# Kernel optimization log

Measured on AMD Instinct MI355X. Metric: run time of the kernel, lower is better.

Reference implementation:

```python
import jax, jax.numpy as jnp
import numpy as np

BITS = 4
GROUP = 128
IN_F = 4096
OUT_F = 4096
N_TOK = 8192
N_STAGES = 4
QMAX = 2 ** BITS - 1  # affine (sym=False)


def _round_ste(x):
    return x + jax.lax.stop_gradient(jnp.round(x) - x)


def _clamp_ste(x, lo, hi):
    return x + jax.lax.stop_gradient(jnp.clip(x, lo, hi) - x)


def apply_rotation(x, pairs, theta, group_size):
    # x: [N, H]; pairs: [R, H] int (per-group index pairs in [0, group_size));
    # theta: [R, H//2]
    n, h = x.shape
    g = h // group_size
    half = group_size // 2
    offsets = (jnp.arange(g, dtype=jnp.int32) * group_size)[:, None]  # [G,1]
    pair_view = pairs.reshape(pairs.shape[0], g, half, 2)
    theta_view = theta.reshape(theta.shape[0], g, half)
    out = x
    for r in range(pairs.shape[0]):  # small fixed number of rotation stages
        idx_i = (pair_view[r, :, :, 0] + offsets).reshape(-1)  # [H//2]
        idx_j = (pair_view[r, :, :, 1] + offsets).reshape(-1)
        xi = out[:, idx_i]  # [N, H//2]
        xj = out[:, idx_j]
        c = jnp.cos(theta_view[r]).reshape(-1)[None, :]
        s = jnp.sin(theta_view[r]).reshape(-1)[None, :]
        out = out.at[:, idx_i].set(xi * c + xj * s).at[:, idx_j].set(-xi * s + xj * c)
    return out


def quant_dequant_affine_ste(w, scale, zero_point_float, group_size):
    # pseudo_quantize_dequant with sym=False, use_ste=True
    view = w.reshape(-1, group_size)
    s = _clamp_ste(scale, 1e-5, 1e5)
    rzp = _clamp_ste(-_round_ste(zero_point_float), 0.0, float(QMAX))
    q = _round_ste(view / s) + rzp
    q = _clamp_ste(q, 0.0, float(QMAX))
    return ((q - rzp) * s).reshape(w.shape)


def setup_inputs() -> dict:
    key = jax.random.key(0)
    k1, k2, k3, k4 = jax.random.split(key, 4)
    x = jax.random.normal(k1, (N_TOK, IN_F), dtype=jnp.float32)
    weight = jax.random.normal(k2, (OUT_F, IN_F), dtype=jnp.float32) * 0.02
    bias = jax.random.normal(k3, (OUT_F,), dtype=jnp.float32) * 0.01
    channel_scales = jnp.ones((IN_F,), dtype=jnp.float32)
    theta = jax.random.normal(k4, (N_STAGES, IN_F // 2), dtype=jnp.float32) * 0.05
    # per-group pair permutations: each stage/group is a permutation of [0, GROUP)
    rng = np.random.default_rng(0)
    g = IN_F // GROUP
    pairs_np = np.stack([
        np.concatenate([rng.permutation(GROUP) for _ in range(g)])
        for _ in range(N_STAGES)
    ]).astype(np.int32)  # [R, IN_F]
    pairs = jnp.asarray(pairs_np)
    # affine qparams from initial (theta=0, scales=1) transformed weight == weight
    view = weight.reshape(-1, GROUP)
    min_val = view.min(axis=1, keepdims=True)
    max_val = view.max(axis=1, keepdims=True)
    q_scale = jnp.clip(max_val - min_val, 1e-5, None) / QMAX
    q_zero_point = min_val / q_scale
    theta_mask = jnp.ones((N_STAGES, IN_F // 2), dtype=bool)
    return {"x": x, "weight": weight, "bias": bias,
            "channel_scales": channel_scales, "theta": theta,
            "q_scale": q_scale, "q_zero_point": q_zero_point,
            "pairs": pairs, "theta_mask": theta_mask}


def reference(x, weight, bias, channel_scales, theta, q_scale, q_zero_point, pairs, theta_mask):
    # transformed_weight(): scale input channels then group-wise Givens rotate
    w_scaled = weight * channel_scales[None, :]
    w_t = apply_rotation(w_scaled, pairs, theta, GROUP)
    # STE pseudo quantize-dequantize in the transformed domain
    w_q = quant_dequant_affine_ste(w_t, q_scale, q_zero_point, GROUP)
    # inverse rotation back to the original input domain, undo channel scales
    w_back = apply_rotation(w_q, pairs[::-1], -theta[::-1], GROUP) / channel_scales[None, :]
    return x @ w_back.T + bias[None, :]
```

## Files before the change

kernel.cpp:

```cpp
#include <hip/hip_runtime.h>
#include <hip/hip_bf16.h>
#include <math.h>

#define IN_F    4096
#define OUT_F   4096
#define N_TOK   8192
#define GROUP   128
#define NSTAGE  4
#define NPAIRS  2048
#define QMAXF   15.0

typedef unsigned short u16;
typedef __bf16 bf16x8 __attribute__((ext_vector_type(8)));
typedef float  f32x4  __attribute__((ext_vector_type(4)));

struct alignas(8) U16x4 { u16 x, y, z, w; };

__device__ __forceinline__ u16 f2bf(float f) {
    unsigned u = __float_as_uint(f);
    unsigned r = (u + 0x7fffu + ((u >> 16) & 1u)) >> 16;
    return (u16)r;
}

__device__ __forceinline__ void gl_lds16(const void* g, void* l) {
    __builtin_amdgcn_global_load_lds(
        (const __attribute__((address_space(1))) void*)g,
        (__attribute__((address_space(3))) void*)l,
        16, 0, 0);
}

__global__ void make_tabs(const float* __restrict__ theta,
                          double* __restrict__ ctab, double* __restrict__ stab) {
    int i = blockIdx.x * 256 + threadIdx.x;
    if (i < NSTAGE * NPAIRS) {
        double t = (double)theta[i];
        ctab[i] = cos(t);
        stab[i] = sin(t);
    }
}

__global__ __launch_bounds__(256) void build_w(
    const float* __restrict__ weight, const float* __restrict__ cs,
    const float* __restrict__ qs, const float* __restrict__ qzp,
    const int* __restrict__ pairs,
    const double* __restrict__ ctab, const double* __restrict__ stab,
    u16* __restrict__ wb) {
    __shared__ double gbuf[4][GROUP];
    const int wave = threadIdx.x >> 6, l = threadIdx.x & 63;
    const int task = blockIdx.x * 4 + wave;
    const int o = task >> 5, g = task & 31;
    double* gb = gbuf[wave];
    const int e0 = g * GROUP;

    float2 wv = *(const float2*)(weight + (size_t)o * IN_F + e0 + 2 * l);
    float2 cv = *(const float2*)(cs + e0 + 2 * l);
    gb[2 * l]     = (double)wv.x * (double)cv.x;
    gb[2 * l + 1] = (double)wv.y * (double)cv.y;
    __builtin_amdgcn_wave_barrier();

    const int2* prs = (const int2*)pairs;

    for (int r = 0; r < NSTAGE; ++r) {
        int2 p = prs[r * (IN_F / 2) + g * 64 + l];
        double c = ctab[r * NPAIRS + g * 64 + l];
        double s = stab[r * NPAIRS + g * 64 + l];
        double xi = gb[p.x], xj = gb[p.y];
        __builtin_amdgcn_wave_barrier();
        gb[p.x] =  xi * c + xj * s;
        gb[p.y] = -xi * s + xj * c;
        __builtin_amdgcn_wave_barrier();
    }

    {
        double s   = fmin(fmax((double)qs[o * 32 + g], 1e-5), 1e5);
        double rzp = fmin(fmax(-rint((double)qzp[o * 32 + g]), 0.0), QMAXF);
#pragma unroll
        for (int e = 2 * l; e <= 2 * l + 1; ++e) {
            double q = rint(gb[e] / s) + rzp;
            q = fmin(fmax(q, 0.0), QMAXF);
            gb[e] = (q - rzp) * s;
        }
        __builtin_amdgcn_wave_barrier();
    }

    for (int r = NSTAGE - 1; r >= 0; --r) {
        int2 p = prs[r * (IN_F / 2) + g * 64 + l];
        double c = ctab[r * NPAIRS + g * 64 + l];
        double s = stab[r * NPAIRS + g * 64 + l];
        double xi = gb[p.x], xj = gb[p.y];
        __builtin_amdgcn_wave_barrier();
        gb[p.x] = xi * c - xj * s;
        gb[p.y] = xi * s + xj * c;
        __builtin_amdgcn_wave_barrier();
    }

    unsigned lo = f2bf((float)(gb[2 * l]     / (double)cv.x));
    unsigned hi = f2bf((float)(gb[2 * l + 1] / (double)cv.y));
    *(unsigned*)(wb + (size_t)o * IN_F + e0 + 2 * l) = lo | (hi << 16);
}

__global__ void cast_x(const float* __restrict__ x, u16* __restrict__ xb) {
    size_t i = ((size_t)blockIdx.x * 256 + threadIdx.x) * 4;
    float4 v = *(const float4*)(x + i);
    U16x4 o;
    o.x = f2bf(v.x); o.y = f2bf(v.y); o.z = f2bf(v.z); o.w = f2bf(v.w);
    *(U16x4*)(xb + i) = o;
}

__global__ __launch_bounds__(256) void gemm_bt(
    const u16* __restrict__ A, const u16* __restrict__ B,
    const float* __restrict__ bias, float* __restrict__ C) {
    constexpr int K = IN_F;
    constexpr int N = OUT_F;
    __shared__ __align__(16) u16 As[128 * 32];
    __shared__ __align__(16) u16 Bs[128 * 32];

    const int tid  = threadIdx.x;
    const int wave = tid >> 6, lane = tid & 63;
    const int ntile = N / 128;
    const int mt = blockIdx.x / ntile, nt = blockIdx.x % ntile;
    const int m0 = mt * 128, n0 = nt * 128;
    const u16* Ab = A + (size_t)m0 * K;
    const u16* Bb = B + (size_t)n0 * K;

    f32x4 acc[4][4];
#pragma unroll
    for (int i = 0; i < 4; ++i)
#pragma unroll
        for (int j = 0; j < 4; ++j) acc[i][j] = (f32x4){0.f, 0.f, 0.f, 0.f};

    const int lrow = lane & 15, lq = lane >> 4;
    const int mw = (wave >> 1) * 64, nw = (wave & 1) * 64;

    const int sc0 = tid;
    const int sc1 = 256 + tid;
    const int srow0 = sc0 >> 2, sgch0 = ((sc0 ^ (srow0 >> 1)) & 3) << 3;
    const int srow1 = sc1 >> 2, sgch1 = ((sc1 ^ (srow1 >> 1)) & 3) << 3;

    for (int k0 = 0; k0 < K; k0 += 32) {
        gl_lds16(Ab + (size_t)srow0 * K + (k0 + sgch0), &As[(wave * 64) * 8]);
        gl_lds16(Ab + (size_t)srow1 * K + (k0 + sgch1), &As[(256 + wave * 64) * 8]);
        gl_lds16(Bb + (size_t)srow0 * K + (k0 + sgch0), &Bs[(wave * 64) * 8]);
        gl_lds16(Bb + (size_t)srow1 * K + (k0 + sgch1), &Bs[(256 + wave * 64) * 8]);
        __syncthreads();

        bf16x8 af[4], bfr[4];
#pragma unroll
        for (int i = 0; i < 4; ++i) {
            int ar = mw + i * 16 + lrow;
            af[i] = *(const bf16x8*)&As[ar * 32 + (((lq ^ (ar >> 1)) & 3) << 3)];
        }
#pragma unroll
        for (int j = 0; j < 4; ++j) {
            int br = nw + j * 16 + lrow;
            bfr[j] = *(const bf16x8*)&Bs[br * 32 + (((lq ^ (br >> 1)) & 3) << 3)];
        }
#pragma unroll
        for (int i = 0; i < 4; ++i)
#pragma unroll
            for (int j = 0; j < 4; ++j)
                acc[i][j] = __builtin_amdgcn_mfma_f32_16x16x32_bf16(
                    af[i], bfr[j], acc[i][j], 0, 0, 0);
        __syncthreads();
    }

#pragma unroll
    for (int i = 0; i < 4; ++i) {
        int rb = m0 + mw + i * 16 + lq * 4;
#pragma unroll
        for (int j = 0; j < 4; ++j) {
            int col = n0 + nw + j * 16 + lrow;
            float bv = bias[col];
#pragma unroll
            for (int r = 0; r < 4; ++r)
                C[(size_t)(rb + r) * N + col] = acc[i][j][r] + bv;
        }
    }
}

extern "C" void kernel_launch(void* const* d_in, const int* in_sizes, int n_in,
                              void* d_out, int out_size, void* d_ws, size_t ws_size,
                              hipStream_t stream) {
    const float* x    = (const float*)d_in[0];
    const float* w    = (const float*)d_in[1];
    const float* bias = (const float*)d_in[2];
    const float* cs   = (const float*)d_in[3];
    const float* th   = (const float*)d_in[4];
    const float* qs   = (const float*)d_in[5];
    const float* qzp  = (const float*)d_in[6];
    const int*   pr   = (const int*)d_in[7];
    float* out = (float*)d_out;

    char* ws = (char*)d_ws;
    double* ctab = (double*)ws;
    double* stab = (double*)(ws + 65536);
    u16*    xb   = (u16*)(ws + 131072);
    u16*    wb   = (u16*)(ws + 131072 + (size_t)N_TOK * IN_F * 2);

    hipLaunchKernelGGL(make_tabs, dim3((NSTAGE * NPAIRS + 255) / 256), dim3(256),
                       0, stream, th, ctab, stab);
    hipLaunchKernelGGL(build_w, dim3(OUT_F * 32 / 4), dim3(256), 0, stream,
                       w, cs, qs, qzp, pr, ctab, stab, wb);
    hipLaunchKernelGGL(cast_x, dim3(N_TOK * IN_F / 4 / 256), dim3(256), 0, stream,
                       x, xb);
    hipLaunchKernelGGL(gemm_bt, dim3((N_TOK / 128) * (OUT_F / 128)), dim3(256),
                       0, stream, xb, wb, bias, out);
}
```

Baseline: 645.2 us.

## Restructure GEMM to 256x256 tiles with 4-stage async LDS pipeline

Rewrites the bf16 GEMM to use 512-thread blocks on 256x256 output tiles, with a four-slot LDS ring that prefetches three k-steps ahead through direct global-to-LDS loads gated by manual vmcnt waits. A single barrier per k-step replaces the two per step used before. It also adds a blockIdx swizzle for L2 locality and raises MFMA priority with setprio. The goal is to hide global load latency and raise arithmetic intensity per block. The cost is a larger LDS footprint (128 KB per block) and more accumulator registers, which may limit occupancy.

```diff
diff --git a/kernel.cpp b/kernel.cpp
--- a/kernel.cpp
+++ b/kernel.cpp
@@ -107,73 +107,97 @@
     *(U16x4*)(xb + i) = o;
 }
 
-__global__ __launch_bounds__(256) void gemm_bt(
+__global__ __launch_bounds__(512, 2) void gemm_bt(
     const u16* __restrict__ A, const u16* __restrict__ B,
     const float* __restrict__ bias, float* __restrict__ C) {
     constexpr int K = IN_F;
     constexpr int N = OUT_F;
-    __shared__ __align__(16) u16 As[128 * 32];
-    __shared__ __align__(16) u16 Bs[128 * 32];
+    constexpr int NS = K / 32;
+    __shared__ __align__(16) u16 As[4][256 * 32];
+    __shared__ __align__(16) u16 Bs[4][256 * 32];
 
     const int tid  = threadIdx.x;
     const int wave = tid >> 6, lane = tid & 63;
-    const int ntile = N / 128;
-    const int mt = blockIdx.x / ntile, nt = blockIdx.x % ntile;
-    const int m0 = mt * 128, n0 = nt * 128;
-    const u16* Ab = A + (size_t)m0 * K;
-    const u16* Bb = B + (size_t)n0 * K;
-
-    f32x4 acc[4][4];
-#pragma unroll
-    for (int i = 0; i < 4; ++i)
+    const int lrow = lane & 15, lq = lane >> 4;
+    const int wm = wave >> 2, wn = wave & 3;
+
+    const int wg = (blockIdx.x & 7) * 64 + (blockIdx.x >> 3);
+    const int mt = wg & 31, nt = wg >> 5;
+    const int m0 = mt * 256, n0 = nt * 256;
+
+    const int srow = tid >> 2;
+    const int gch  = (tid & 3) ^ ((tid >> 3) & 3);
+    const u16* pA0 = A + (size_t)(m0 + srow) * K + gch * 8;
+    const u16* pA1 = pA0 + (size_t)128 * K;
+    const u16* pB0 = B + (size_t)(n0 + srow) * K + gch * 8;
+    const u16* pB1 = pB0 + (size_t)128 * K;
+
+#define STAGE(slot, s) do {                                         \
+        const int ko_ = (s) * 32;                                   \
+        gl_lds16(pA0 + ko_, &As[slot][wave * 512]);                 \
+        gl_lds16(pA1 + ko_, &As[slot][4096 + wave * 512]);          \
+        gl_lds16(pB0 + ko_, &Bs[slot][wave * 512]);                 \
+        gl_lds16(pB1 + ko_, &Bs[slot][4096 + wave * 512]);          \
+    } while (0)
+
+    f32x4 acc[8][4];
+#pragma unroll
+    for (int i = 0; i < 8; ++i)
 #pragma unroll
         for (int j = 0; j < 4; ++j) acc[i][j] = (f32x4){0.f, 0.f, 0.f, 0.f};
 
-    const int lrow = lane & 15, lq = lane >> 4;
-    const int mw = (wave >> 1) * 64, nw = (wave & 1) * 64;
-
-    const int sc0 = tid;
-    const int sc1 = 256 + tid;
-    const int srow0 = sc0 >> 2, sgch0 = ((sc0 ^ (srow0 >> 1)) & 3) << 3;
-    const int srow1 = sc1 >> 2, sgch1 = ((sc1 ^ (srow1 >> 1)) & 3) << 3;
-
-    for (int k0 = 0; k0 < K; k0 += 32) {
-        gl_lds16(Ab + (size_t)srow0 * K + (k0 + sgch0), &As[(wave * 64) * 8]);
-        gl_lds16(Ab + (size_t)srow1 * K + (k0 + sgch1), &As[(256 + wave * 64) * 8]);
-        gl_lds16(Bb + (size_t)srow0 * K + (k0 + sgch0), &Bs[(wave * 64) * 8]);
-        gl_lds16(Bb + (size_t)srow1 * K + (k0 + sgch1), &Bs[(256 + wave * 64) * 8]);
-        __syncthreads();
-
-        bf16x8 af[4], bfr[4];
-#pragma unroll
-        for (int i = 0; i < 4; ++i) {
-            int ar = mw + i * 16 + lrow;
-            af[i] = *(const bf16x8*)&As[ar * 32 + (((lq ^ (ar >> 1)) & 3) << 3)];
-        }
-#pragma unroll
-        for (int j = 0; j < 4; ++j) {
-            int br = nw + j * 16 + lrow;
-            bfr[j] = *(const bf16x8*)&Bs[br * 32 + (((lq ^ (br >> 1)) & 3) << 3)];
-        }
-#pragma unroll
-        for (int i = 0; i < 4; ++i)
-#pragma unroll
-            for (int j = 0; j < 4; ++j)
-                acc[i][j] = __builtin_amdgcn_mfma_f32_16x16x32_bf16(
-                    af[i], bfr[j], acc[i][j], 0, 0, 0);
-        __syncthreads();
-    }
-
-#pragma unroll
-    for (int i = 0; i < 4; ++i) {
-        int rb = m0 + mw + i * 16 + lq * 4;
-#pragma unroll
-        for (int j = 0; j < 4; ++j) {
-            int col = n0 + nw + j * 16 + lrow;
+    STAGE(0, 0); STAGE(1, 1); STAGE(2, 2);
+
+#define BODY(s, VMSTR, DO_STAGE) do {                                          \
+        asm volatile("s_waitcnt " VMSTR);                                      \
+        __builtin_amdgcn_s_barrier();                                          \
+        asm volatile("" ::: "memory");                                         \
+        const u16* as_ = As[(s) & 3];                                          \
+        const u16* bs_ = Bs[(s) & 3];                                          \
+        bf16x8 af[8], bf[4];                                                   \
+        _Pragma("unroll")                                                      \
+        for (int mi = 0; mi < 8; ++mi) {                                       \
+            int ar = wm * 128 + mi * 16 + lrow;                                \
+            af[mi] = *(const bf16x8*)&as_[ar * 32 +                            \
+                                          (((lq ^ (ar >> 1)) & 3) << 3)];      \
+        }                                                                      \
+        _Pragma("unroll")                                                      \
+        for (int nj = 0; nj < 4; ++nj) {                                       \
+            int br = wn * 64 + nj * 16 + lrow;                                 \
+            bf[nj] = *(const bf16x8*)&bs_[br * 32 +                            \
+                                          (((lq ^ (br >> 1)) & 3) << 3)];      \
+        }                                                                      \
+        if (DO_STAGE) STAGE(((s) + 3) & 3, (s) + 3);                           \
+        __builtin_amdgcn_s_setprio(1);                                         \
+        _Pragma("unroll")                                                      \
+        for (int mi = 0; mi < 8; ++mi)                                         \
+            _Pragma("unroll")                                                  \
+            for (int nj = 0; nj < 4; ++nj)                                     \
+                acc[mi][nj] = __builtin_amdgcn_mfma_f32_16x16x32_bf16(         \
+                    af[mi], bf[nj], acc[mi][nj], 0, 0, 0);                     \
+        __builtin_amdgcn_s_setprio(0);                                         \
+        asm volatile("" ::: "memory");                                         \
+    } while (0)
+
+    for (int s = 0; s < NS - 3; ++s)
+        BODY(s, "vmcnt(8)", 1);
+    BODY(NS - 3, "vmcnt(8)", 0);
+    BODY(NS - 2, "vmcnt(4)", 0);
+    BODY(NS - 1, "vmcnt(0)", 0);
+
+#undef BODY
+#undef STAGE
+
+#pragma unroll
+    for (int mi = 0; mi < 8; ++mi) {
+        int rb = m0 + wm * 128 + mi * 16 + lq * 4;
+#pragma unroll
+        for (int nj = 0; nj < 4; ++nj) {
+            int col = n0 + wn * 64 + nj * 16 + lrow;
             float bv = bias[col];
 #pragma unroll
             for (int r = 0; r < 4; ++r)
-                C[(size_t)(rb + r) * N + col] = acc[i][j][r] + bv;
+                C[(size_t)(rb + r) * N + col] = acc[mi][nj][r] + bv;
         }
     }
 }
@@ -203,6 +227,6 @@
                        w, cs, qs, qzp, pr, ctab, stab, wb);
     hipLaunchKernelGGL(cast_x, dim3(N_TOK * IN_F / 4 / 256), dim3(256), 0, stream,
                        x, xb);
-    hipLaunchKernelGGL(gemm_bt, dim3((N_TOK / 128) * (OUT_F / 128)), dim3(256),
+    hipLaunchKernelGGL(gemm_bt, dim3((N_TOK / 256) * (OUT_F / 256)), dim3(512),
                        0, stream, xb, wb, bias, out);
 }
```

Result: no change. 634.9 us (-1.6%).
